# Optimization experiments

Measured on AMD Instinct MI355X. Metric: run time of the kernel, lower is better.

The kernel has to match this reference:

```python
import jax, jax.numpy as jnp
import numpy as np

DIM = 96
GROUPS = 8          # SPPE factor
CG = DIM // GROUPS  # channels per SPPE group = 12
D_STATE = 16
D_CONV = 4
D_INNER = 2 * DIM   # expand=2
DT_RANK = 6         # ceil(96/16)
EPS = 1e-5


def setup_inputs() -> dict:
    key = jax.random.key(0)
    ks = jax.random.split(key, 16)
    def w(k, shape, s=0.02):
        return (jax.random.normal(k, shape) * s).astype(jnp.float32)
    z = lambda *s: jnp.zeros(s, jnp.float32)
    inp = {
        "x": jax.random.normal(ks[0], (2, DIM, 32, 32, 32), dtype=jnp.float32),
        # SPPE params
        "sppe_c1_w": w(ks[1], (CG, CG)), "sppe_c1_b": z(CG),
        "sppe_c3_w": w(ks[2], (CG, CG, 3, 3, 3)), "sppe_c3_b": z(CG),
        "sppe_gn_w": jnp.ones((CG,), jnp.float32), "sppe_gn_b": z(CG),
        # Mamba params (mamba_ssm defaults: proj biases False, conv bias True)
        "in_proj_w": w(ks[3], (2 * D_INNER, DIM)),
        "conv1d_w": w(ks[4], (D_INNER, D_CONV), 0.1), "conv1d_b": z(D_INNER),
        "x_proj_w": w(ks[5], (DT_RANK + 2 * D_STATE, D_INNER)),
        "dt_proj_w": w(ks[6], (D_INNER, DT_RANK), 0.1),
        "dt_proj_b": w(ks[7], (D_INNER,), 0.1),
        "A_log": jnp.log(jnp.tile(jnp.arange(1, D_STATE + 1, dtype=jnp.float32), (D_INNER, 1))),
        "ssm_D": jnp.ones((D_INNER,), jnp.float32),
        "out_proj_w": w(ks[8], (DIM, D_INNER)),
        # MlpChannel params (1x1 Conv3d == pointwise linear over channels)
        "mlp_fc1_w": w(ks[9], (4 * DIM, DIM)), "mlp_fc1_b": z(4 * DIM),
        "mlp_fc2_w": w(ks[10], (DIM, 4 * DIM)), "mlp_fc2_b": z(DIM),
    }
    return inp


def _inorm(x):
    # InstanceNorm3d (affine=False, biased var) over spatial dims per (b,c)
    m = jnp.mean(x, axis=(2, 3, 4), keepdims=True)
    v = jnp.var(x, axis=(2, 3, 4), keepdims=True)
    return (x - m) * jax.lax.rsqrt(v + EPS)


def _sppe(x, c1_w, c1_b, c3_w, c3_b, gn_w, gn_b):
    b, c, h, w, d = x.shape
    bg = b * GROUPS
    gx = x.reshape(bg, CG, h, w, d)
    # directional pools, each ending as (bg, CG, axis_len, 1, 1)
    x_h = jnp.mean(gx, axis=(3, 4), keepdims=True)                      # (bg,CG,h,1,1)
    x_w = jnp.mean(gx, axis=(2, 4), keepdims=True).transpose(0, 1, 3, 2, 4)
    x_d = jnp.mean(gx, axis=(2, 3), keepdims=True).transpose(0, 1, 4, 3, 2)
    hwd = jnp.concatenate([x_h, x_w, x_d], axis=2)[..., 0, 0]          # (bg,CG,h+w+d)
    hwd = jnp.einsum("oc,bcn->bon", c1_w, hwd) + c1_b[:, None]
    g_h = jax.nn.sigmoid(hwd[:, :, :h])[:, :, :, None, None]           # (bg,CG,h,1,1)
    g_w = jax.nn.sigmoid(hwd[:, :, h:h + w])[:, :, None, :, None]      # (bg,CG,1,w,1)
    g_d = jax.nn.sigmoid(hwd[:, :, h + w:])[:, :, None, None, :]       # (bg,CG,1,1,d)
    gated = gx * g_h * g_w * g_d
    # GroupNorm(num_groups=CG, num_channels=CG) == per-channel norm + affine
    gm = jnp.mean(gated, axis=(2, 3, 4), keepdims=True)
    gv = jnp.var(gated, axis=(2, 3, 4), keepdims=True)
    x1 = (gated - gm) * jax.lax.rsqrt(gv + EPS)
    x1 = x1 * gn_w[:, None, None, None] + gn_b[:, None, None, None]
    x2 = jax.lax.conv_general_dilated(
        gx, c3_w, (1, 1, 1), [(1, 1)] * 3,
        dimension_numbers=("NCDHW", "OIDHW", "NCDHW")) + c3_b[:, None, None, None]
    n = h * w * d
    x11 = jax.nn.softmax(jnp.mean(x1, axis=(2, 3, 4)), axis=-1)        # (bg,CG)
    x21 = jax.nn.softmax(jnp.mean(x2, axis=(2, 3, 4)), axis=-1)
    x12 = x2.reshape(bg, CG, n)
    x22 = x1.reshape(bg, CG, n)
    weights = (jnp.einsum("bc,bcn->bn", x11, x12)
               + jnp.einsum("bc,bcn->bn", x21, x22)).reshape(bg, 1, h, w, d)
    return (gx * jax.nn.sigmoid(weights)).reshape(b, c, h, w, d)


def _mamba(seq, in_proj_w, conv1d_w, conv1d_b, x_proj_w, dt_proj_w, dt_proj_b,
           A_log, ssm_D, out_proj_w):
    # seq: (B, L, DIM)
    B, L, _ = seq.shape
    xz = seq @ in_proj_w.T                       # (B,L,2*E)
    xm, zg = jnp.split(xz, 2, axis=-1)
    # depthwise causal conv1d along L
    xc = jax.lax.conv_general_dilated(
        xm.transpose(0, 2, 1), conv1d_w[:, None, :], (1,), [(D_CONV - 1, 0)],
        dimension_numbers=("NCH", "OIH", "NCH"), feature_group_count=D_INNER)
    xc = jax.nn.silu((xc + conv1d_b[:, None]).transpose(0, 2, 1))  # (B,L,E)
    dbl = xc @ x_proj_w.T                         # (B,L,DT_RANK+2N)
    dt = jax.nn.softplus(dbl[..., :DT_RANK] @ dt_proj_w.T + dt_proj_b)  # (B,L,E)
    Bm = dbl[..., DT_RANK:DT_RANK + D_STATE]      # (B,L,N)
    Cm = dbl[..., DT_RANK + D_STATE:]             # (B,L,N)
    A = -jnp.exp(A_log)                           # (E,N)

    def step(h, t):
        dt_t, b_t, c_t, x_t = t                   # (B,E),(B,N),(B,N),(B,E)
        dA = jnp.exp(dt_t[:, :, None] * A)        # (B,E,N)
        h = h * dA + (dt_t * x_t)[:, :, None] * b_t[:, None, :]
        return h, jnp.einsum("ben,bn->be", h, c_t)

    h0 = jnp.zeros((B, D_INNER, D_STATE), seq.dtype)
    _, ys = jax.lax.scan(step, h0, (dt.transpose(1, 0, 2), Bm.transpose(1, 0, 2),
                                    Cm.transpose(1, 0, 2), xc.transpose(1, 0, 2)))
    y = ys.transpose(1, 0, 2) + xc * ssm_D
    y = y * jax.nn.silu(zg)
    return y @ out_proj_w.T                       # (B,L,DIM)


def reference(x, sppe_c1_w, sppe_c1_b, sppe_c3_w, sppe_c3_b, sppe_gn_w, sppe_gn_b,
              in_proj_w, conv1d_w, conv1d_b, x_proj_w, dt_proj_w, dt_proj_b,
              A_log, ssm_D, out_proj_w, mlp_fc1_w, mlp_fc1_b, mlp_fc2_w, mlp_fc2_b):
    y_sppe = _sppe(x, sppe_c1_w, sppe_c1_b, sppe_c3_w, sppe_c3_b, sppe_gn_w, sppe_gn_b)
    B, C, H, W, Dd = x.shape
    L = H * W * Dd
    seq = _inorm(x).reshape(B, C, L).transpose(0, 2, 1)           # (B,L,C)
    out = _mamba(seq, in_proj_w, conv1d_w, conv1d_b, x_proj_w,
                 dt_proj_w, dt_proj_b, A_log, ssm_D, out_proj_w)
    xo = out.transpose(0, 2, 1).reshape(B, C, H, W, Dd)
    xo = _inorm(xo) * y_sppe
    t = jnp.einsum("oc,bchwd->bohwd", mlp_fc1_w, xo) + mlp_fc1_b[:, None, None, None]
    t = jax.nn.gelu(t, approximate=False)
    t = jnp.einsum("oc,bchwd->bohwd", mlp_fc2_w, t) + mlp_fc2_b[:, None, None, None]
    return t + x
```

## Files before the change

kernel.cpp:

```cpp
#include <hip/hip_runtime.h>
#include <math.h>

#define NSPA 32768
#define TCH 128
#define NCH 256
#define EPS 1e-5f

#define ST_MEAN   0
#define ST_RSTD   192
#define ST_GM     384
#define ST_GRSTD  576
#define ST_X2SUM  768
#define ST_XH     1024
#define ST_XW     7168
#define ST_XD     13312
#define ST_GATE   19456
#define ST_MEAN2  38400
#define ST_RSTD2  38592
#define ST_WT     40960

__device__ __forceinline__ float sigmoidf_(float x){ return 1.f/(1.f+__expf(-x)); }
__device__ __forceinline__ float siluf_(float x){ return x/(1.f+__expf(-x)); }
__device__ __forceinline__ float geluf_(float x){ return 0.5f*x*(1.f+erff(x*0.70710678118654752f)); }
__device__ __forceinline__ float softplusf_(float x){ return fmaxf(x,0.f) + log1pf(__expf(-fabsf(x))); }

__global__ void k_stats(const float* __restrict__ x, float* __restrict__ st) {
  int bc = blockIdx.x;
  int t = threadIdx.x;
  __shared__ float xh_s[32], xw_s[32], xd_s[32], red[16], red2[16];
  if (t < 32) { xh_s[t]=0.f; xw_s[t]=0.f; xd_s[t]=0.f; }
  __syncthreads();
  const float* px = x + (size_t)bc*NSPA;
  float s=0.f, s2=0.f;
  for (int it=0; it<32; ++it) {
    float v = px[it*1024 + t];
    s += v; s2 += v*v;
    float wv = v;
    #pragma unroll
    for (int m=32;m>=1;m>>=1) wv += __shfl_xor(wv,m);
    if ((t&63)==0) atomicAdd(&xh_s[it], wv);
  }
  atomicAdd(&xw_s[(t>>5)&31], s);
  atomicAdd(&xd_s[t&31], s);
  float rs=s, rs2=s2;
  #pragma unroll
  for (int m=32;m>=1;m>>=1){ rs += __shfl_xor(rs,m); rs2 += __shfl_xor(rs2,m); }
  if ((t&63)==0){ red[t>>6]=rs; red2[t>>6]=rs2; }
  __syncthreads();
  if (t==0){
    float S=0.f,S2=0.f;
    for (int w=0;w<16;w++){ S+=red[w]; S2+=red2[w]; }
    float mn = S/(float)NSPA;
    float var = S2/(float)NSPA - mn*mn;
    st[ST_MEAN+bc] = mn;
    st[ST_RSTD+bc] = rsqrtf(var+EPS);
  }
  if (t<32){
    st[ST_XH + bc*32 + t] = xh_s[t]*(1.f/1024.f);
    st[ST_XW + bc*32 + t] = xw_s[t]*(1.f/1024.f);
    st[ST_XD + bc*32 + t] = xd_s[t]*(1.f/1024.f);
  }
}

__global__ void k_gates(const float* __restrict__ c1w, const float* __restrict__ c1b,
                        float* __restrict__ st) {
  int bg = blockIdx.x; int b = bg>>3; int g = bg&7;
  for (int i = threadIdx.x; i < 12*96; i += 128) {
    int co = i/96, pos = i%96;
    float acc = c1b[co];
    for (int cg=0; cg<12; ++cg) {
      int bc = b*96 + g*12 + cg;
      float hv;
      if (pos < 32)      hv = st[ST_XH + bc*32 + pos];
      else if (pos < 64) hv = st[ST_XW + bc*32 + pos-32];
      else               hv = st[ST_XD + bc*32 + pos-64];
      acc += c1w[co*12+cg]*hv;
    }
    st[ST_GATE + bg*1152 + i] = sigmoidf_(acc);
  }
}

__global__ void k_gated(const float* __restrict__ x, float* __restrict__ gated,
                        float* __restrict__ st) {
  int bc = blockIdx.x; int bg = bc/12; int cg = bc%12;
  int t = threadIdx.x;
  const float* gate = st + ST_GATE + bg*1152 + cg*96;
  float gw = gate[32 + (t>>5)];
  float gd = gate[64 + (t&31)];
  const float* px = x + (size_t)bc*NSPA;
  float* pg = gated + (size_t)bc*NSPA;
  __shared__ float red[16], red2[16];
  float s=0.f, s2=0.f;
  for (int it=0; it<32; ++it) {
    float gh = gate[it];
    float v = px[it*1024+t]*gh*gw*gd;
    pg[it*1024+t] = v;
    s += v; s2 += v*v;
  }
  #pragma unroll
  for (int m=32;m>=1;m>>=1){ s += __shfl_xor(s,m); s2 += __shfl_xor(s2,m); }
  if ((t&63)==0){ red[t>>6]=s; red2[t>>6]=s2; }
  __syncthreads();
  if (t==0){
    float S=0.f,S2=0.f;
    for (int w=0;w<16;w++){ S+=red[w]; S2+=red2[w]; }
    float mn = S/(float)NSPA;
    float var = S2/(float)NSPA - mn*mn;
    st[ST_GM+bc] = mn;
    st[ST_GRSTD+bc] = rsqrtf(var+EPS);
  }
}

__global__ void k_wt(const float* __restrict__ c3w, float* __restrict__ wt) {
  int idx = blockIdx.x*256 + threadIdx.x;
  if (idx >= 3888) return;
  int co = idx/324, r = idx%324;
  wt[r*12 + co] = c3w[co*324 + r];
}

__global__ void k_w1t(const float* __restrict__ W1, float* __restrict__ W1t) {
  int idx = blockIdx.x*256 + threadIdx.x;
  if (idx >= 384*96) return;
  int k = idx/384, h = idx%384;
  W1t[idx] = W1[(size_t)h*96 + k];
}
__global__ void k_w2t(const float* __restrict__ W2, float* __restrict__ W2t) {
  int idx = blockIdx.x*256 + threadIdx.x;
  if (idx >= 384*96) return;
  int k = idx/96, o = idx%96;
  W2t[idx] = W2[(size_t)o*384 + k];
}

__global__ void k_conv3(const float* __restrict__ x, const float* __restrict__ wt,
                        const float* __restrict__ c3b, float* __restrict__ x2,
                        float* __restrict__ st) {
  __shared__ float sl[3][12*324];
  __shared__ float ssum[12];
  int bg = blockIdx.z;
  int w0 = (blockIdx.x & 1)*16, d0 = (blockIdx.x >> 1)*16;
  int h0 = blockIdx.y*4;
  int tid = threadIdx.x;
  if (tid < 12) ssum[tid] = 0.f;

  const float* xb = x + (size_t)bg*12*NSPA;

  auto load_slab = [&](int hh, int s){
    for (int i=tid; i<3888; i+=256){
      int ci = i/324, r = i%324;
      int lw = r/18, ld = r%18;
      int gw = w0-1+lw, gd = d0-1+ld;
      float v = 0.f;
      if ((unsigned)hh<32u && (unsigned)gw<32u && (unsigned)gd<32u)
        v = xb[(size_t)ci*NSPA + hh*1024 + gw*32 + gd];
      sl[s][i] = v;
    }
  };

  load_slab(h0-1, ((h0-1)%3+3)%3);
  load_slab(h0,   h0%3);
  load_slab(h0+1, (h0+1)%3);
  __syncthreads();

  int w = tid>>4, d = tid&15;
  int base_wd = w*18 + d;
  float b0v=c3b[0],b1v=c3b[1],b2v=c3b[2],b3v=c3b[3],b4v=c3b[4],b5v=c3b[5],
        b6v=c3b[6],b7v=c3b[7],b8v=c3b[8],b9v=c3b[9],b10v=c3b[10],b11v=c3b[11];

  for (int it=0; it<4; ++it){
    int h = h0 + it;
    const float* sm1 = sl[((h-1)%3+3)%3];
    const float* s00 = sl[h%3];
    const float* sp1 = sl[(h+1)%3];
    float acc[12];
    acc[0]=b0v; acc[1]=b1v; acc[2]=b2v; acc[3]=b3v; acc[4]=b4v; acc[5]=b5v;
    acc[6]=b6v; acc[7]=b7v; acc[8]=b8v; acc[9]=b9v; acc[10]=b10v; acc[11]=b11v;
    for (int ci=0; ci<12; ++ci){
      const float* w_ci = wt + ci*324;
      #pragma unroll
      for (int kh=0;kh<3;kh++){
        const float* sp = (kh==0)? sm1 : ((kh==1)? s00 : sp1);
        const float* srow = sp + ci*324 + base_wd;
        #pragma unroll
        for (int kw=0;kw<3;kw++){
          #pragma unroll
          for (int kd=0;kd<3;kd++){
            float v = srow[kw*18 + kd];
            const float4* wp = (const float4*)(w_ci + (kh*9+kw*3+kd)*12);
            float4 wa = wp[0], wb = wp[1], wc = wp[2];
            acc[0]=fmaf(wa.x,v,acc[0]); acc[1]=fmaf(wa.y,v,acc[1]);
            acc[2]=fmaf(wa.z,v,acc[2]); acc[3]=fmaf(wa.w,v,acc[3]);
            acc[4]=fmaf(wb.x,v,acc[4]); acc[5]=fmaf(wb.y,v,acc[5]);
            acc[6]=fmaf(wb.z,v,acc[6]); acc[7]=fmaf(wb.w,v,acc[7]);
            acc[8]=fmaf(wc.x,v,acc[8]); acc[9]=fmaf(wc.y,v,acc[9]);
            acc[10]=fmaf(wc.z,v,acc[10]); acc[11]=fmaf(wc.w,v,acc[11]);
          }
        }
      }
    }
    int l = h*1024 + (w0+w)*32 + (d0+d);
    #pragma unroll
    for (int co=0;co<12;co++){
      float r = acc[co];
      x2[(size_t)(bg*12+co)*NSPA + l] = r;
      float rv = r;
      #pragma unroll
      for (int m=32;m>=1;m>>=1) rv += __shfl_xor(rv,m);
      if ((tid&63)==0) atomicAdd(&ssum[co], rv);
    }
    __syncthreads();
    if (it<3){
      load_slab(h+2, (h+2)%3);
      __syncthreads();
    }
  }
  if (tid<12) atomicAdd(&st[ST_X2SUM + bg*12 + tid], ssum[tid]);
}

__global__ void k_sppe_out(const float* __restrict__ x, const float* __restrict__ gated,
                           const float* __restrict__ x2, const float* __restrict__ gnw,
                           const float* __restrict__ gnb, const float* __restrict__ st,
                           float* __restrict__ ysppe) {
  int bg = blockIdx.y; int b = bg>>3; int g = bg&7;
  __shared__ float x11s[12], alphas[12], betasum_s;
  if (threadIdx.x==0){
    float m1=-1e30f, m2=-1e30f;
    float mu2[12];
    for (int cg=0;cg<12;cg++){
      int bc=b*96+g*12+cg;
      mu2[cg] = st[ST_X2SUM+bc]*(1.f/(float)NSPA);
      m1 = fmaxf(m1, gnb[cg]); m2 = fmaxf(m2, mu2[cg]);
    }
    float e1[12], e2[12]; float s1=0.f, s2=0.f;
    for (int cg=0;cg<12;cg++){ e1[cg]=expf(gnb[cg]-m1); s1+=e1[cg];
                               e2[cg]=expf(mu2[cg]-m2); s2+=e2[cg]; }
    float bs=0.f;
    for (int cg=0;cg<12;cg++){
      int bc=b*96+g*12+cg;
      float x11 = e1[cg]/s1;
      float x21 = e2[cg]/s2;
      x11s[cg]=x11;
      float gr = st[ST_GRSTD+bc], gm = st[ST_GM+bc];
      alphas[cg] = x21*gr*gnw[cg];
      bs += x21*(gnb[cg] - gm*gr*gnw[cg]);
    }
    betasum_s = bs;
  }
  __syncthreads();
  int l = blockIdx.x*256 + threadIdx.x;
  float wsum = betasum_s;
  int bc0 = b*96+g*12;
  for (int cg=0;cg<12;cg++){
    size_t off = (size_t)(bc0+cg)*NSPA + l;
    wsum += x11s[cg]*x2[off] + alphas[cg]*gated[off];
  }
  float sig = sigmoidf_(wsum);
  for (int cg=0;cg<12;cg++){
    size_t off = (size_t)(bc0+cg)*NSPA + l;
    ysppe[off] = x[off]*sig;
  }
}

__global__ void k_gemm_in(const float* __restrict__ A, const float* __restrict__ W,
                          float* __restrict__ xm_t, float* __restrict__ zg_t,
                          const float* __restrict__ mean, const float* __restrict__ rstd) {
  __shared__ float As[96*64];
  int b = blockIdx.y; int l0 = blockIdx.x*64; int tid = threadIdx.x;
  for (int i=tid;i<96*64;i+=256){
    int k=i>>6, l=i&63;
    float v = A[((size_t)b*96+k)*NSPA + l0+l];
    As[i] = (v-mean[b*96+k])*rstd[b*96+k];
  }
  __syncthreads();
  int l4=(tid&15)*4; int og=tid>>4;
  for (int o0=og*4; o0<384; o0+=64){
    float acc[16];
    #pragma unroll
    for (int i=0;i<16;i++) acc[i]=0.f;
    for (int k=0;k<96;k++){
      float4 a = *(const float4*)&As[k*64+l4];
      #pragma unroll
      for (int j=0;j<4;j++){
        float wv = W[(size_t)(o0+j)*96+k];
        acc[j*4+0]+=wv*a.x; acc[j*4+1]+=wv*a.y; acc[j*4+2]+=wv*a.z; acc[j*4+3]+=wv*a.w;
      }
    }
    #pragma unroll
    for (int i=0;i<4;i++){
      int l = l0+l4+i;
      float4 r; r.x=acc[0*4+i]; r.y=acc[1*4+i]; r.z=acc[2*4+i]; r.w=acc[3*4+i];
      if (o0 < 192) *(float4*)&xm_t[((size_t)b*NSPA + l)*192 + o0] = r;
      else          *(float4*)&zg_t[((size_t)b*NSPA + l)*192 + (o0-192)] = r;
    }
  }
}

__global__ void k_conv1d_t(const float* __restrict__ xm_t, const float* __restrict__ cw,
                           const float* __restrict__ cb, float* __restrict__ xc_t) {
  int b = blockIdx.y; int l0 = blockIdx.x*128; int e = threadIdx.x;
  float4 w4 = *(const float4*)&cw[e*4];
  float bias = cb[e];
  const float* base = xm_t + (size_t)b*NSPA*192 + e;
  float* out = xc_t + (size_t)b*NSPA*192 + e;
  float hm3 = (l0>0) ? base[(size_t)(l0-3)*192] : 0.f;
  float hm2 = (l0>0) ? base[(size_t)(l0-2)*192] : 0.f;
  float hm1 = (l0>0) ? base[(size_t)(l0-1)*192] : 0.f;
  for (int l=0;l<128;l++){
    float cur = base[(size_t)(l0+l)*192];
    float acc = bias + w4.x*hm3 + w4.y*hm2 + w4.z*hm1 + w4.w*cur;
    out[(size_t)(l0+l)*192] = siluf_(acc);
    hm3=hm2; hm2=hm1; hm1=cur;
  }
}

__global__ void k_gemm_xp(const float* __restrict__ A, const float* __restrict__ W,
                          float* __restrict__ dbl_t) {
  __shared__ float As[192*64];
  int b = blockIdx.y; int l0 = blockIdx.x*64; int tid = threadIdx.x;
  for (int f=tid; f<48*64; f+=256){
    int l = f&63, kq = f>>6;
    float4 v = *(const float4*)&A[((size_t)b*NSPA + l0+l)*192 + kq*4];
    As[(kq*4+0)*64+l]=v.x; As[(kq*4+1)*64+l]=v.y;
    As[(kq*4+2)*64+l]=v.z; As[(kq*4+3)*64+l]=v.w;
  }
  __syncthreads();
  int l4=(tid&15)*4; int og=tid>>4;
  for (int o0=og*4; o0<40; o0+=64){
    float acc[16];
    #pragma unroll
    for (int i=0;i<16;i++) acc[i]=0.f;
    for (int k=0;k<192;k++){
      float4 a = *(const float4*)&As[k*64+l4];
      #pragma unroll
      for (int j=0;j<4;j++){
        int o = o0+j;
        int row = (o<32) ? (o+6) : (o-32);
        float wv = (o<38) ? W[(size_t)row*192+k] : 0.f;
        acc[j*4+0]+=wv*a.x; acc[j*4+1]+=wv*a.y; acc[j*4+2]+=wv*a.z; acc[j*4+3]+=wv*a.w;
      }
    }
    #pragma unroll
    for (int i=0;i<4;i++){
      int l = l0+l4+i;
      float4 r; r.x=acc[0*4+i]; r.y=acc[1*4+i]; r.z=acc[2*4+i]; r.w=acc[3*4+i];
      *(float4*)&dbl_t[((size_t)b*NSPA + l)*40 + o0] = r;
    }
  }
}

__global__ void k_gemm_out(const float* __restrict__ A, const float* __restrict__ W,
                           float* __restrict__ out) {
  __shared__ float As[192*64];
  int b = blockIdx.y; int l0 = blockIdx.x*64; int tid = threadIdx.x;
  for (int f=tid; f<48*64; f+=256){
    int l = f&63, kq = f>>6;
    float4 v = *(const float4*)&A[((size_t)b*NSPA + l0+l)*192 + kq*4];
    As[(kq*4+0)*64+l]=v.x; As[(kq*4+1)*64+l]=v.y;
    As[(kq*4+2)*64+l]=v.z; As[(kq*4+3)*64+l]=v.w;
  }
  __syncthreads();
  int l4=(tid&15)*4; int og=tid>>4;
  for (int o0=og*4; o0<96; o0+=64){
    float acc[16];
    #pragma unroll
    for (int i=0;i<16;i++) acc[i]=0.f;
    for (int k=0;k<192;k++){
      float4 a = *(const float4*)&As[k*64+l4];
      #pragma unroll
      for (int j=0;j<4;j++){
        float wv = W[(size_t)(o0+j)*192+k];
        acc[j*4+0]+=wv*a.x; acc[j*4+1]+=wv*a.y; acc[j*4+2]+=wv*a.z; acc[j*4+3]+=wv*a.w;
      }
    }
    #pragma unroll
    for (int j=0;j<4;j++){
      int o=o0+j;
      float4 r; r.x=acc[j*4+0]; r.y=acc[j*4+1]; r.z=acc[j*4+2]; r.w=acc[j*4+3];
      *(float4*)&out[((size_t)b*96+o)*NSPA + l0+l4] = r;
    }
  }
}

__global__ void k_scanA(const float* __restrict__ xc_t, const float* __restrict__ dbl_t,
                        const float* __restrict__ dtw, const float* __restrict__ dtb,
                        const float* __restrict__ A_log,
                        float* __restrict__ P, float* __restrict__ hend) {
  int b = blockIdx.y, ch = blockIdx.x; int e = threadIdx.x;
  float An[16];
  #pragma unroll
  for (int n=0;n<16;n++) An[n] = -__expf(A_log[e*16+n]);
  float wdt[6];
  #pragma unroll
  for (int j=0;j<6;j++) wdt[j]=dtw[e*6+j];
  float bdt = dtb[e];
  const float* drow = dbl_t + ((size_t)b*NSPA + (size_t)ch*TCH)*40;
  const float* xrow = xc_t + ((size_t)b*NSPA + (size_t)ch*TCH)*192 + e;
  float h[16], Pp[16];
  #pragma unroll
  for (int n=0;n<16;n++){ h[n]=0.f; Pp[n]=1.f; }
  for (int l=0;l<TCH;l++){
    const float* u = drow + l*40;
    float4 b0=*(const float4*)(u+0), b1=*(const float4*)(u+4),
           b2=*(const float4*)(u+8), b3=*(const float4*)(u+12);
    float4 d4=*(const float4*)(u+32);
    float2 d2=*(const float2*)(u+36);
    float x = xrow[(size_t)l*192];
    float pre = bdt + wdt[0]*d4.x + wdt[1]*d4.y + wdt[2]*d4.z
                    + wdt[3]*d4.w + wdt[4]*d2.x + wdt[5]*d2.y;
    float dte = softplusf_(pre);
    float dtx = dte*x;
    float Bv[16] = {b0.x,b0.y,b0.z,b0.w, b1.x,b1.y,b1.z,b1.w,
                    b2.x,b2.y,b2.z,b2.w, b3.x,b3.y,b3.z,b3.w};
    #pragma unroll
    for (int n=0;n<16;n++){
      float a = __expf(dte*An[n]);
      Pp[n] *= a;
      h[n] = h[n]*a + dtx*Bv[n];
    }
  }
  size_t o = (((size_t)b*NCH+ch)*192+e)*16;
  #pragma unroll
  for (int q=0;q<4;q++){
    float4 rp; rp.x=Pp[q*4+0]; rp.y=Pp[q*4+1]; rp.z=Pp[q*4+2]; rp.w=Pp[q*4+3];
    *(float4*)&P[o+q*4] = rp;
    float4 rh; rh.x=h[q*4+0]; rh.y=h[q*4+1]; rh.z=h[q*4+2]; rh.w=h[q*4+3];
    *(float4*)&hend[o+q*4] = rh;
  }
}

__global__ void k_scanB(const float* __restrict__ P, const float* __restrict__ hend,
                        float* __restrict__ Hs) {
  int t = blockIdx.x*256 + threadIdx.x;
  int b = t / 3072; int r = t % 3072;
  size_t base = (size_t)b*NCH*3072 + r;
  float H = 0.f;
  float Pc = P[base], Hc = hend[base];
  for (int c=0;c<NCH;c++){
    size_t idx = base + (size_t)c*3072;
    float Pn=0.f, Hn=0.f;
    if (c+1<NCH){ Pn = P[idx+3072]; Hn = hend[idx+3072]; }
    Hs[idx] = H;
    H = fmaf(Pc, H, Hc);
    Pc = Pn; Hc = Hn;
  }
}

__global__ void k_scanC(const float* xc_t, const float* __restrict__ dbl_t,
                        const float* __restrict__ dtw, const float* __restrict__ dtb,
                        const float* __restrict__ A_log, const float* __restrict__ Hs,
                        const float* __restrict__ ssm_D, const float* __restrict__ zg_t,
                        float* y_t) {
  int b = blockIdx.y, ch = blockIdx.x; int e = threadIdx.x;
  float An[16];
  #pragma unroll
  for (int n=0;n<16;n++) An[n] = -__expf(A_log[e*16+n]);
  float wdt[6];
  #pragma unroll
  for (int j=0;j<6;j++) wdt[j]=dtw[e*6+j];
  float bdt = dtb[e];
  float Dv = ssm_D[e];
  const float* drow = dbl_t + ((size_t)b*NSPA + (size_t)ch*TCH)*40;
  const float* xrow = xc_t + ((size_t)b*NSPA + (size_t)ch*TCH)*192 + e;
  const float* zrow = zg_t + ((size_t)b*NSPA + (size_t)ch*TCH)*192 + e;
  float* yrow = y_t + ((size_t)b*NSPA + (size_t)ch*TCH)*192 + e;
  float h[16];
  size_t ho = (((size_t)b*NCH+ch)*192+e)*16;
  #pragma unroll
  for (int q=0;q<4;q++){
    float4 hv = *(const float4*)&Hs[ho+q*4];
    h[q*4+0]=hv.x; h[q*4+1]=hv.y; h[q*4+2]=hv.z; h[q*4+3]=hv.w;
  }
  for (int l=0;l<TCH;l++){
    const float* u = drow + l*40;
    float4 b0=*(const float4*)(u+0), b1=*(const float4*)(u+4),
           b2=*(const float4*)(u+8), b3=*(const float4*)(u+12);
    float4 c0=*(const float4*)(u+16), c1=*(const float4*)(u+20),
           c2=*(const float4*)(u+24), c3=*(const float4*)(u+28);
    float4 d4=*(const float4*)(u+32);
    float2 d2=*(const float2*)(u+36);
    float x = xrow[(size_t)l*192];
    float z = zrow[(size_t)l*192];
    float pre = bdt + wdt[0]*d4.x + wdt[1]*d4.y + wdt[2]*d4.z
                    + wdt[3]*d4.w + wdt[4]*d2.x + wdt[5]*d2.y;
    float dte = softplusf_(pre);
    float dtx = dte*x;
    float Bv[16] = {b0.x,b0.y,b0.z,b0.w, b1.x,b1.y,b1.z,b1.w,
                    b2.x,b2.y,b2.z,b2.w, b3.x,b3.y,b3.z,b3.w};
    float Cv[16] = {c0.x,c0.y,c0.z,c0.w, c1.x,c1.y,c1.z,c1.w,
                    c2.x,c2.y,c2.z,c2.w, c3.x,c3.y,c3.z,c3.w};
    float yp = 0.f;
    #pragma unroll
    for (int n=0;n<16;n++){
      float a = __expf(dte*An[n]);
      h[n] = h[n]*a + dtx*Bv[n];
      yp += h[n]*Cv[n];
    }
    yrow[(size_t)l*192] = (yp + x*Dv)*siluf_(z);
  }
}

__global__ void k_stats2(const float* __restrict__ outb, float* __restrict__ st) {
  int bc = blockIdx.x; int t = threadIdx.x;
  const float* p = outb + (size_t)bc*NSPA;
  float s=0.f, s2=0.f;
  for (int i=t;i<NSPA;i+=256){ float v=p[i]; s+=v; s2+=v*v; }
  __shared__ float red[4], red2[4];
  #pragma unroll
  for (int m=32;m>=1;m>>=1){ s += __shfl_xor(s,m); s2 += __shfl_xor(s2,m); }
  if ((t&63)==0){ red[t>>6]=s; red2[t>>6]=s2; }
  __syncthreads();
  if (t==0){
    float S=red[0]+red[1]+red[2]+red[3];
    float S2=red2[0]+red2[1]+red2[2]+red2[3];
    float mn=S/(float)NSPA; float var=S2/(float)NSPA-mn*mn;
    st[ST_MEAN2+bc]=mn; st[ST_RSTD2+bc]=rsqrtf(var+EPS);
  }
}

__global__ void k_mlpF(const float* __restrict__ outb, const float* __restrict__ ysppe,
                       const float* __restrict__ st,
                       const float* __restrict__ W1t, const float* __restrict__ b1,
                       const float* __restrict__ W2t, const float* __restrict__ b2,
                       const float* __restrict__ x, float* __restrict__ dout) {
  __shared__ float xoS[96*64];
  __shared__ float hidS[64*64];
  int b = blockIdx.y; int l0 = blockIdx.x*64; int tid = threadIdx.x;
  for (int i=tid;i<96*64;i+=256){
    int k=i>>6, l=i&63;
    size_t off = ((size_t)b*96+k)*NSPA + l0+l;
    xoS[i] = (outb[off]-st[ST_MEAN2+b*96+k])*st[ST_RSTD2+b*96+k]*ysppe[off];
  }
  __syncthreads();
  int wv = __builtin_amdgcn_readfirstlane(tid >> 6);
  int lane = tid & 63;
  float acc2[24];
  #pragma unroll
  for (int i=0;i<24;i++) acc2[i]=0.f;
  int o0 = wv*24;

  for (int c=0; c<6; ++c){
    int h0 = c*64 + wv*16;
    float acc1[16];
    #pragma unroll
    for (int i=0;i<16;i++) acc1[i]=0.f;
    for (int k=0;k<96;k++){
      float a = xoS[k*64 + lane];
      const float4* wp = (const float4*)&W1t[(size_t)k*384 + h0];
      float4 w0=wp[0], w1=wp[1], w2=wp[2], w3=wp[3];
      acc1[0]=fmaf(w0.x,a,acc1[0]);  acc1[1]=fmaf(w0.y,a,acc1[1]);
      acc1[2]=fmaf(w0.z,a,acc1[2]);  acc1[3]=fmaf(w0.w,a,acc1[3]);
      acc1[4]=fmaf(w1.x,a,acc1[4]);  acc1[5]=fmaf(w1.y,a,acc1[5]);
      acc1[6]=fmaf(w1.z,a,acc1[6]);  acc1[7]=fmaf(w1.w,a,acc1[7]);
      acc1[8]=fmaf(w2.x,a,acc1[8]);  acc1[9]=fmaf(w2.y,a,acc1[9]);
      acc1[10]=fmaf(w2.z,a,acc1[10]); acc1[11]=fmaf(w2.w,a,acc1[11]);
      acc1[12]=fmaf(w3.x,a,acc1[12]); acc1[13]=fmaf(w3.y,a,acc1[13]);
      acc1[14]=fmaf(w3.z,a,acc1[14]); acc1[15]=fmaf(w3.w,a,acc1[15]);
    }
    if (c) __syncthreads();
    #pragma unroll
    for (int j=0;j<16;j++)
      hidS[(wv*16+j)*64 + lane] = geluf_(acc1[j] + b1[h0+j]);
    __syncthreads();
    for (int k2=0;k2<64;k2++){
      float a = hidS[k2*64 + lane];
      int kg = c*64 + k2;
      const float4* wp = (const float4*)&W2t[(size_t)kg*96 + o0];
      float4 w0=wp[0], w1=wp[1], w2=wp[2], w3=wp[3], w4=wp[4], w5=wp[5];
      acc2[0]=fmaf(w0.x,a,acc2[0]);  acc2[1]=fmaf(w0.y,a,acc2[1]);
      acc2[2]=fmaf(w0.z,a,acc2[2]);  acc2[3]=fmaf(w0.w,a,acc2[3]);
      acc2[4]=fmaf(w1.x,a,acc2[4]);  acc2[5]=fmaf(w1.y,a,acc2[5]);
      acc2[6]=fmaf(w1.z,a,acc2[6]);  acc2[7]=fmaf(w1.w,a,acc2[7]);
      acc2[8]=fmaf(w2.x,a,acc2[8]);  acc2[9]=fmaf(w2.y,a,acc2[9]);
      acc2[10]=fmaf(w2.z,a,acc2[10]); acc2[11]=fmaf(w2.w,a,acc2[11]);
      acc2[12]=fmaf(w3.x,a,acc2[12]); acc2[13]=fmaf(w3.y,a,acc2[13]);
      acc2[14]=fmaf(w3.z,a,acc2[14]); acc2[15]=fmaf(w3.w,a,acc2[15]);
      acc2[16]=fmaf(w4.x,a,acc2[16]); acc2[17]=fmaf(w4.y,a,acc2[17]);
      acc2[18]=fmaf(w4.z,a,acc2[18]); acc2[19]=fmaf(w4.w,a,acc2[19]);
      acc2[20]=fmaf(w5.x,a,acc2[20]); acc2[21]=fmaf(w5.y,a,acc2[21]);
      acc2[22]=fmaf(w5.z,a,acc2[22]); acc2[23]=fmaf(w5.w,a,acc2[23]);
    }
  }
  #pragma unroll
  for (int j=0;j<24;j++){
    int o = o0 + j;
    size_t off = ((size_t)b*96+o)*NSPA + l0 + lane;
    dout[off] = acc2[j] + b2[o] + x[off];
  }
}

extern "C" void kernel_launch(void* const* d_in, const int* in_sizes, int n_in,
                              void* d_out, int out_size, void* d_ws, size_t ws_size,
                              hipStream_t stream) {
  const float* x        = (const float*)d_in[0];
  const float* c1w      = (const float*)d_in[1];
  const float* c1b      = (const float*)d_in[2];
  const float* c3w      = (const float*)d_in[3];
  const float* c3b      = (const float*)d_in[4];
  const float* gnw      = (const float*)d_in[5];
  const float* gnb      = (const float*)d_in[6];
  const float* in_proj  = (const float*)d_in[7];
  const float* conv1dw  = (const float*)d_in[8];
  const float* conv1db  = (const float*)d_in[9];
  const float* xprojw   = (const float*)d_in[10];
  const float* dtw      = (const float*)d_in[11];
  const float* dtb      = (const float*)d_in[12];
  const float* A_log    = (const float*)d_in[13];
  const float* ssm_D    = (const float*)d_in[14];
  const float* outprojw = (const float*)d_in[15];
  const float* W1       = (const float*)d_in[16];
  const float* b1       = (const float*)d_in[17];
  const float* W2       = (const float*)d_in[18];
  const float* b2       = (const float*)d_in[19];
  float* dout = (float*)d_out;

  float* ws = (float*)d_ws;
  const size_t o_st = 0;
  const size_t o_A  = 65536;
  const size_t o_B  = o_A + 12582912;
  const size_t o_C  = o_B + 12582912;
  const size_t o_D  = o_C + 12582912;
  const size_t o_E  = o_D + 6291456;
  const size_t o_F  = o_E + 6291456;
  float* st    = ws + o_st;
  float* xm_t  = ws + o_A;
  float* Hs    = ws + o_A;
  float* W1t   = ws + o_A + 1600000;
  float* W2t   = ws + o_A + 1700000;
  float* zg_t  = ws + o_B;
  float* xc_t  = ws + o_C;
  float* y_t   = ws + o_C;
  float* gated = ws + o_D;
  float* dbl_t = ws + o_D;
  float* P     = ws + o_D + 2621440;
  float* hend  = ws + o_D + 2621440 + 1572864;
  float* x2b   = ws + o_E;
  float* outb  = ws + o_E;
  float* ysppe = ws + o_F;
  float* wtb   = st + ST_WT;

  hipMemsetAsync(st, 0, 65536*sizeof(float), stream);

  k_stats<<<192, 1024, 0, stream>>>(x, st);
  k_gates<<<16, 128, 0, stream>>>(c1w, c1b, st);
  k_gated<<<192, 1024, 0, stream>>>(x, gated, st);
  k_wt<<<16, 256, 0, stream>>>(c3w, wtb);
  k_conv3<<<dim3(4,8,16), 256, 0, stream>>>(x, wtb, c3b, x2b, st);
  k_sppe_out<<<dim3(128,16), 256, 0, stream>>>(x, gated, x2b, gnw, gnb, st, ysppe);
  k_gemm_in<<<dim3(512,2), 256, 0, stream>>>(x, in_proj, xm_t, zg_t,
                                             st+ST_MEAN, st+ST_RSTD);
  k_conv1d_t<<<dim3(256,2), 192, 0, stream>>>(xm_t, conv1dw, conv1db, xc_t);
  k_w1t<<<144, 256, 0, stream>>>(W1, W1t);
  k_w2t<<<144, 256, 0, stream>>>(W2, W2t);
  k_gemm_xp<<<dim3(512,2), 256, 0, stream>>>(xc_t, xprojw, dbl_t);
  k_scanA<<<dim3(NCH,2), 192, 0, stream>>>(xc_t, dbl_t, dtw, dtb, A_log, P, hend);
  k_scanB<<<24, 256, 0, stream>>>(P, hend, Hs);
  k_scanC<<<dim3(NCH,2), 192, 0, stream>>>(xc_t, dbl_t, dtw, dtb, A_log, Hs,
                                           ssm_D, zg_t, y_t);
  k_gemm_out<<<dim3(512,2), 256, 0, stream>>>(y_t, outprojw, outb);
  k_stats2<<<192, 256, 0, stream>>>(outb, st);
  k_mlpF<<<dim3(512,2), 256, 0, stream>>>(outb, ysppe, st, W1t, b1, W2t, b2, x, dout);
}
```

Before: 949.8 us.

## Shrink scan chunks, parallelize inter-chunk scan, halve conv1d and MLP tiles

Scan chunk length drops from 128 to 32, so there are 1024 chunks and scanA/scanC launch four times as many blocks. scanB becomes a two-level scan: 16 groups of 64 chunks are each reduced in parallel, combined through shared memory, then rescanned. conv1d blocks now cover 64 positions each, and the MLP hidden tile shrinks from 64 to 32 to cut register and LDS use. Workspace buffers are moved to fit the larger P/hend arrays, and scanB reads P and hend from global memory twice.

```diff
diff --git a/kernel.cpp b/kernel.cpp
--- a/kernel.cpp
+++ b/kernel.cpp
@@ -2,8 +2,8 @@
 #include <math.h>
 
 #define NSPA 32768
-#define TCH 128
-#define NCH 256
+#define TCH 32
+#define NCH 1024
 #define EPS 1e-5f
 
 #define ST_MEAN   0
@@ -296,7 +296,7 @@
 
 __global__ void k_conv1d_t(const float* __restrict__ xm_t, const float* __restrict__ cw,
                            const float* __restrict__ cb, float* __restrict__ xc_t) {
-  int b = blockIdx.y; int l0 = blockIdx.x*128; int e = threadIdx.x;
+  int b = blockIdx.y; int l0 = blockIdx.x*64; int e = threadIdx.x;
   float4 w4 = *(const float4*)&cw[e*4];
   float bias = cb[e];
   const float* base = xm_t + (size_t)b*NSPA*192 + e;
@@ -304,7 +304,7 @@
   float hm3 = (l0>0) ? base[(size_t)(l0-3)*192] : 0.f;
   float hm2 = (l0>0) ? base[(size_t)(l0-2)*192] : 0.f;
   float hm1 = (l0>0) ? base[(size_t)(l0-1)*192] : 0.f;
-  for (int l=0;l<128;l++){
+  for (int l=0;l<64;l++){
     float cur = base[(size_t)(l0+l)*192];
     float acc = bias + w4.x*hm3 + w4.y*hm2 + w4.z*hm1 + w4.w*cur;
     out[(size_t)(l0+l)*192] = siluf_(acc);
@@ -429,18 +429,29 @@
 
 __global__ void k_scanB(const float* __restrict__ P, const float* __restrict__ hend,
                         float* __restrict__ Hs) {
-  int t = blockIdx.x*256 + threadIdx.x;
-  int b = t / 3072; int r = t % 3072;
+  __shared__ float sP[16][64], sH[16][64];
+  int b = blockIdx.y;
+  int rl = threadIdx.x & 63;
+  int cg = threadIdx.x >> 6;
+  int r  = blockIdx.x*64 + rl;
   size_t base = (size_t)b*NCH*3072 + r;
+  int c0 = cg*64;
+  float Pl = 1.f, hl = 0.f;
+  for (int c=c0; c<c0+64; ++c){
+    size_t idx = base + (size_t)c*3072;
+    float Pc = P[idx], Hc = hend[idx];
+    hl = fmaf(Pc, hl, Hc);
+    Pl *= Pc;
+  }
+  sP[cg][rl] = Pl; sH[cg][rl] = hl;
+  __syncthreads();
   float H = 0.f;
-  float Pc = P[base], Hc = hend[base];
-  for (int c=0;c<NCH;c++){
+  for (int g=0; g<cg; ++g) H = fmaf(sP[g][rl], H, sH[g][rl]);
+  for (int c=c0; c<c0+64; ++c){
     size_t idx = base + (size_t)c*3072;
-    float Pn=0.f, Hn=0.f;
-    if (c+1<NCH){ Pn = P[idx+3072]; Hn = hend[idx+3072]; }
+    float Pc = P[idx], Hc = hend[idx];
     Hs[idx] = H;
     H = fmaf(Pc, H, Hc);
-    Pc = Pn; Hc = Hn;
   }
 }
 
@@ -522,7 +533,7 @@
                        const float* __restrict__ W2t, const float* __restrict__ b2,
                        const float* __restrict__ x, float* __restrict__ dout) {
   __shared__ float xoS[96*64];
-  __shared__ float hidS[64*64];
+  __shared__ float hidS[32*64];
   int b = blockIdx.y; int l0 = blockIdx.x*64; int tid = threadIdx.x;
   for (int i=tid;i<96*64;i+=256){
     int k=i>>6, l=i&63;
@@ -537,32 +548,28 @@
   for (int i=0;i<24;i++) acc2[i]=0.f;
   int o0 = wv*24;
 
-  for (int c=0; c<6; ++c){
-    int h0 = c*64 + wv*16;
-    float acc1[16];
-    #pragma unroll
-    for (int i=0;i<16;i++) acc1[i]=0.f;
+  for (int c=0; c<12; ++c){
+    int h0 = c*32 + wv*8;
+    float acc1[8];
+    #pragma unroll
+    for (int i=0;i<8;i++) acc1[i]=0.f;
     for (int k=0;k<96;k++){
       float a = xoS[k*64 + lane];
       const float4* wp = (const float4*)&W1t[(size_t)k*384 + h0];
-      float4 w0=wp[0], w1=wp[1], w2=wp[2], w3=wp[3];
+      float4 w0=wp[0], w1=wp[1];
       acc1[0]=fmaf(w0.x,a,acc1[0]);  acc1[1]=fmaf(w0.y,a,acc1[1]);
       acc1[2]=fmaf(w0.z,a,acc1[2]);  acc1[3]=fmaf(w0.w,a,acc1[3]);
       acc1[4]=fmaf(w1.x,a,acc1[4]);  acc1[5]=fmaf(w1.y,a,acc1[5]);
       acc1[6]=fmaf(w1.z,a,acc1[6]);  acc1[7]=fmaf(w1.w,a,acc1[7]);
-      acc1[8]=fmaf(w2.x,a,acc1[8]);  acc1[9]=fmaf(w2.y,a,acc1[9]);
-      acc1[10]=fmaf(w2.z,a,acc1[10]); acc1[11]=fmaf(w2.w,a,acc1[11]);
-      acc1[12]=fmaf(w3.x,a,acc1[12]); acc1[13]=fmaf(w3.y,a,acc1[13]);
-      acc1[14]=fmaf(w3.z,a,acc1[14]); acc1[15]=fmaf(w3.w,a,acc1[15]);
     }
     if (c) __syncthreads();
     #pragma unroll
-    for (int j=0;j<16;j++)
-      hidS[(wv*16+j)*64 + lane] = geluf_(acc1[j] + b1[h0+j]);
+    for (int j=0;j<8;j++)
+      hidS[(wv*8+j)*64 + lane] = geluf_(acc1[j] + b1[h0+j]);
     __syncthreads();
-    for (int k2=0;k2<64;k2++){
+    for (int k2=0;k2<32;k2++){
       float a = hidS[k2*64 + lane];
-      int kg = c*64 + k2;
+      int kg = c*32 + k2;
       const float4* wp = (const float4*)&W2t[(size_t)kg*96 + o0];
       float4 w0=wp[0], w1=wp[1], w2=wp[2], w3=wp[3], w4=wp[4], w5=wp[5];
       acc2[0]=fmaf(w0.x,a,acc2[0]);  acc2[1]=fmaf(w0.y,a,acc2[1]);
@@ -622,17 +629,17 @@
   const size_t o_F  = o_E + 6291456;
   float* st    = ws + o_st;
   float* xm_t  = ws + o_A;
-  float* Hs    = ws + o_A;
-  float* W1t   = ws + o_A + 1600000;
-  float* W2t   = ws + o_A + 1700000;
+  float* P     = ws + o_A;
+  float* Hs    = ws + o_A + 6291456;
   float* zg_t  = ws + o_B;
   float* xc_t  = ws + o_C;
   float* y_t   = ws + o_C;
   float* gated = ws + o_D;
   float* dbl_t = ws + o_D;
-  float* P     = ws + o_D + 2621440;
-  float* hend  = ws + o_D + 2621440 + 1572864;
+  float* W1t   = ws + o_D + 3000000;
+  float* W2t   = ws + o_D + 3100000;
   float* x2b   = ws + o_E;
+  float* hendb = ws + o_E;
   float* outb  = ws + o_E;
   float* ysppe = ws + o_F;
   float* wtb   = st + ST_WT;
@@ -647,12 +654,12 @@
   k_sppe_out<<<dim3(128,16), 256, 0, stream>>>(x, gated, x2b, gnw, gnb, st, ysppe);
   k_gemm_in<<<dim3(512,2), 256, 0, stream>>>(x, in_proj, xm_t, zg_t,
                                              st+ST_MEAN, st+ST_RSTD);
-  k_conv1d_t<<<dim3(256,2), 192, 0, stream>>>(xm_t, conv1dw, conv1db, xc_t);
+  k_conv1d_t<<<dim3(512,2), 192, 0, stream>>>(xm_t, conv1dw, conv1db, xc_t);
   k_w1t<<<144, 256, 0, stream>>>(W1, W1t);
   k_w2t<<<144, 256, 0, stream>>>(W2, W2t);
   k_gemm_xp<<<dim3(512,2), 256, 0, stream>>>(xc_t, xprojw, dbl_t);
-  k_scanA<<<dim3(NCH,2), 192, 0, stream>>>(xc_t, dbl_t, dtw, dtb, A_log, P, hend);
-  k_scanB<<<24, 256, 0, stream>>>(P, hend, Hs);
+  k_scanA<<<dim3(NCH,2), 192, 0, stream>>>(xc_t, dbl_t, dtw, dtb, A_log, P, hendb);
+  k_scanB<<<dim3(48,2), 1024, 0, stream>>>(P, hendb, Hs);
   k_scanC<<<dim3(NCH,2), 192, 0, stream>>>(xc_t, dbl_t, dtw, dtb, A_log, Hs,
                                            ssm_D, zg_t, y_t);
   k_gemm_out<<<dim3(512,2), 256, 0, stream>>>(y_t, outprojw, outb);
```

After: 888.3 us. -6.5%, faster.
